# Kernel optimization log

Measured on AMD Instinct MI355X. Metric: run time of the kernel, lower is better.

Reference implementation:

```python
import jax, jax.numpy as jnp
import numpy as np

DIM = 1024        # BIGNET_DIM
GS = 16           # group_size
N_LAYERS = 18     # 6 blocks * 3 QLoRALinear
N_BLOCKS = 6
R = 32            # lora_dim
B = 32768         # flattened batch/tokens
LN_EPS = 1e-5


def _qlora_linear(x, qw, sc, b, la, lb):
    # Dequantize int4 weights: per-group (group_size=16 along in_features) scale.
    O, I = qw.shape
    w = (qw.astype(jnp.float32).reshape(O, I // GS, GS) * sc[:, :, None]).reshape(O, I)
    base = x @ w.T + b                      # [B, O] dequant-matmul
    lora = (x @ la.T) @ lb.T                # fp32 low-rank branch [B,R]->[B,O]
    return base + lora


def _layernorm(x, g, b):
    mu = jnp.mean(x, axis=-1, keepdims=True)
    var = jnp.mean((x - mu) ** 2, axis=-1, keepdims=True)
    return (x - mu) * jax.lax.rsqrt(var + LN_EPS) * g + b


def setup_inputs() -> dict:
    key = jax.random.key(0)
    ks = jax.random.split(key, 6)
    x = jax.random.normal(ks[0], (B, DIM), dtype=jnp.float32)
    # int4 codes in [-8, 7]
    qw = jax.random.randint(ks[1], (N_LAYERS, DIM, DIM), -8, 8, dtype=jnp.int32)
    # positive per-group scales (absmax/7-like magnitude)
    scales = jax.random.uniform(ks[2], (N_LAYERS, DIM, DIM // GS), dtype=jnp.float32,
                                minval=0.005, maxval=0.02)
    bias = 0.02 * jax.random.normal(ks[3], (N_LAYERS, DIM), dtype=jnp.float32)
    lora_a = (1.0 / np.sqrt(DIM)) * jax.random.normal(ks[4], (N_LAYERS, R, DIM), dtype=jnp.float32)
    # lora_b is zero-init in the module; use small random values so the branch is exercised
    lora_b = 0.01 * jax.random.normal(ks[5], (N_LAYERS, DIM, R), dtype=jnp.float32)
    ln_g = jnp.ones((N_BLOCKS - 1, DIM), dtype=jnp.float32)
    ln_b = jnp.zeros((N_BLOCKS - 1, DIM), dtype=jnp.float32)
    return {"x": x, "qw": qw, "scales": scales, "bias": bias,
            "lora_a": lora_a, "lora_b": lora_b, "ln_g": ln_g, "ln_b": ln_b}


def reference(x, qw, scales, bias, lora_a, lora_b, ln_g, ln_b):
    h = x
    for blk in range(N_BLOCKS):
        y = h
        for j in range(3):
            li = blk * 3 + j
            y = _qlora_linear(y, qw[li], scales[li], bias[li], lora_a[li], lora_b[li])
            if j < 2:
                y = jax.nn.relu(y)
        h = y + h                     # residual
        if blk < N_BLOCKS - 1:
            h = _layernorm(h, ln_g[blk], ln_b[blk])
    return h
```

## Files before the change

kernel.cpp:

```cpp
#include <hip/hip_runtime.h>
#include <cstdint>

typedef _Float16 f16;
typedef _Float16 f16x8 __attribute__((ext_vector_type(8)));
typedef _Float16 f16x4 __attribute__((ext_vector_type(4)));
typedef float    f32x4 __attribute__((ext_vector_type(4)));
typedef float    f32x16 __attribute__((ext_vector_type(16)));

#define DIMN 1024
#define BATCH 32768
#define NLAYERS 18
#define NBLOCKS 6

__device__ __forceinline__ void gl2lds16(const f16* g, const f16* l) {
    auto gp = (const __attribute__((address_space(1))) unsigned int*)(uintptr_t)g;
    auto lp = (__attribute__((address_space(3))) unsigned int*)(uintptr_t)l;
    __builtin_amdgcn_global_load_lds(gp, lp, 16, 0, 0);
}

__global__ void cvt_kernel(const float* __restrict__ x, f16* __restrict__ o) {
    int i = (blockIdx.x * 256 + threadIdx.x) * 4;
    float4 v = *(const float4*)&x[i];
    f16x4 r;
    r[0] = (f16)v.x; r[1] = (f16)v.y; r[2] = (f16)v.z; r[3] = (f16)v.w;
    *(f16x4*)&o[i] = r;
}

__global__ __launch_bounds__(256) void prep_w_kernel(
        const int* __restrict__ qw, const float* __restrict__ sc,
        const float* __restrict__ la, const float* __restrict__ lb,
        f16* __restrict__ W) {
    int b = blockIdx.x;
    int li = b >> 7;
    int og = (b & 127) << 3;
    __shared__ float lbs[8][32];
    int tid = threadIdx.x;
    lbs[tid >> 5][tid & 31] = lb[((size_t)li * 1024 + og + (tid >> 5)) * 32 + (tid & 31)];
    __syncthreads();

    int i0 = tid * 4;
    const float* laL = la + (size_t)li * 32 * 1024;
    float acc[8][4] = {};
    for (int r = 0; r < 32; ++r) {
        float4 lav = *(const float4*)&laL[r * 1024 + i0];
#pragma unroll
        for (int q = 0; q < 8; ++q) {
            float wv = lbs[q][r];
            acc[q][0] += wv * lav.x; acc[q][1] += wv * lav.y;
            acc[q][2] += wv * lav.z; acc[q][3] += wv * lav.w;
        }
    }
#pragma unroll
    for (int q = 0; q < 8; ++q) {
        size_t row = (size_t)li * 1024 + og + q;
        size_t rowbase = row * 1024;
        int4 code = *(const int4*)&qw[rowbase + i0];
        float scale = sc[row * 64 + (i0 >> 4)];
        f16x4 o;
        o[0] = (f16)((float)code.x * scale + acc[q][0]);
        o[1] = (f16)((float)code.y * scale + acc[q][1]);
        o[2] = (f16)((float)code.z * scale + acc[q][2]);
        o[3] = (f16)((float)code.w * scale + acc[q][3]);
        *(f16x4*)&W[rowbase + i0] = o;
    }
}

__global__ __launch_bounds__(512, 2) void gemm_kernel(
        const f16* __restrict__ A, const f16* __restrict__ W,
        const float* __restrict__ bias, f16* __restrict__ C, int relu) {
    __shared__ __align__(16) char smem[131072];

    int tid = threadIdx.x;
    int l = tid & 63, w = tid >> 6;
    int wm = w >> 2, wn = w & 3;
    int m_l = l & 31;
    int kg = l >> 5;

    int hb = blockIdx.x;
    int xcd = hb & 7, idx = hb >> 3;
    int mt = xcd * 16 + (idx >> 2);
    int nt = idx & 3;
    int bm = mt * 256, bn = nt * 256;

    int R0 = tid >> 3;
    int lgc = (tid & 7) ^ (R0 & 7);
    int hh = lgc >> 2, kch = lgc & 3;
    const f16* pA = A + (size_t)(bm + hh * 128 + R0) * 1024 + kch * 8;
    const f16* pB = W + (size_t)(bn + hh * 128 + R0) * 1024 + kch * 8;
    int ld0 = tid * 16;

#define STGA(SL, KT) do { \
    gl2lds16(pA + (KT) * 32, (const f16*)(smem + (SL) * 32768 + ld0)); \
    gl2lds16(pA + 65536 + (KT) * 32, (const f16*)(smem + (SL) * 32768 + 8192 + ld0)); } while (0)
#define STGB(SL, KT) do { \
    gl2lds16(pB + (KT) * 32, (const f16*)(smem + (SL) * 32768 + 16384 + ld0)); \
    gl2lds16(pB + 65536 + (KT) * 32, (const f16*)(smem + (SL) * 32768 + 24576 + ld0)); } while (0)

    int aoff[4], boff[2];
#pragma unroll
    for (int mf = 0; mf < 4; ++mf) aoff[mf] = (mf * 32 + m_l) * 128;
#pragma unroll
    for (int nf = 0; nf < 2; ++nf) boff[nf] = 16384 + ((wn & 1) * 64 + nf * 32 + m_l) * 128;
    int r7 = m_l & 7;
    int sa0 = ((wm * 4 + 0 + kg) ^ r7) * 16;
    int sa1 = ((wm * 4 + 2 + kg) ^ r7) * 16;
    int sb0 = (((wn >> 1) * 4 + 0 + kg) ^ r7) * 16;
    int sb1 = (((wn >> 1) * 4 + 2 + kg) ^ r7) * 16;

    f16x8 aE[4], bE[2], aO[4], bO[2];
    f32x16 acc[4][2] = {};

#define READS(DA, DB, SBASE, SA, SB) do { _Pragma("unroll") \
    for (int mf = 0; mf < 4; ++mf) DA[mf] = *(const f16x8*)(smem + (SBASE) + aoff[mf] + (SA)); \
    _Pragma("unroll") \
    for (int nf = 0; nf < 2; ++nf) DB[nf] = *(const f16x8*)(smem + (SBASE) + boff[nf] + (SB)); } while (0)

#define MMA8(AF, BF) do { _Pragma("unroll") \
    for (int mf = 0; mf < 4; ++mf) { _Pragma("unroll") \
      for (int nf = 0; nf < 2; ++nf) \
        acc[mf][nf] = __builtin_amdgcn_mfma_f32_32x32x16_f16(BF[nf], AF[mf], acc[mf][nf], 0, 0, 0); } } while (0)

#define WAITS do { \
    asm volatile("s_waitcnt vmcnt(4) lgkmcnt(6)" ::: "memory"); \
    __builtin_amdgcn_sched_barrier(0); \
    __builtin_amdgcn_s_barrier(); \
    __builtin_amdgcn_sched_barrier(0); } while (0)

#define PHASES(T4, DT) do { \
    int kp = ((T4) + (DT) + 3) & 31; \
     \
    READS(aO, bO, ((DT) & 3) * 32768, sa1, sb1); \
    STGA(((DT) + 3) & 3, kp); \
    WAITS; \
    __builtin_amdgcn_s_setprio(1); \
    MMA8(aE, bE); \
    __builtin_amdgcn_s_setprio(0); \
    __builtin_amdgcn_sched_barrier(0); \
     \
    READS(aE, bE, (((DT) + 1) & 3) * 32768, sa0, sb0); \
    STGB(((DT) + 3) & 3, kp); \
    WAITS; \
    __builtin_amdgcn_s_setprio(1); \
    MMA8(aO, bO); \
    __builtin_amdgcn_s_setprio(0); \
    __builtin_amdgcn_sched_barrier(0); \
  } while (0)

    STGA(0, 0); STGB(0, 0);
    STGA(1, 1); STGB(1, 1);
    STGA(2, 2); STGB(2, 2);
    asm volatile("s_waitcnt vmcnt(4)" ::: "memory");
    __builtin_amdgcn_s_barrier();
    READS(aE, bE, 0, sa0, sb0);

#pragma unroll 1
    for (int t4 = 0; t4 < 32; t4 += 4) {
        PHASES(t4, 0);
        PHASES(t4, 1);
        PHASES(t4, 2);
        PHASES(t4, 3);
    }

    __syncthreads();
    f16* Cs = (f16*)smem;
    float4 bsv[2][4];
#pragma unroll
    for (int nf = 0; nf < 2; ++nf)
#pragma unroll
        for (int g = 0; g < 4; ++g)
            bsv[nf][g] = *(const float4*)&bias[bn + wn * 64 + nf * 32 + g * 8 + kg * 4];

    int c8 = (tid & 31) * 8, rr = tid >> 5;
#pragma unroll
    for (int pass = 0; pass < 2; ++pass) {
        if (wm == pass) {
#pragma unroll
            for (int mf = 0; mf < 4; ++mf) {
                int row = mf * 32 + m_l;
#pragma unroll
                for (int nf = 0; nf < 2; ++nf)
#pragma unroll
                    for (int g = 0; g < 4; ++g) {
                        float4 vb = bsv[nf][g];
                        float v0 = acc[mf][nf][g * 4 + 0] + vb.x;
                        float v1 = acc[mf][nf][g * 4 + 1] + vb.y;
                        float v2 = acc[mf][nf][g * 4 + 2] + vb.z;
                        float v3 = acc[mf][nf][g * 4 + 3] + vb.w;
                        if (relu) {
                            v0 = fmaxf(v0, 0.f); v1 = fmaxf(v1, 0.f);
                            v2 = fmaxf(v2, 0.f); v3 = fmaxf(v3, 0.f);
                        }
                        f16x4 pk;
                        pk[0] = (f16)v0; pk[1] = (f16)v1; pk[2] = (f16)v2; pk[3] = (f16)v3;
                        *(f16x4*)&Cs[row * 264 + wn * 64 + nf * 32 + g * 8 + kg * 4] = pk;
                    }
            }
        }
        __syncthreads();
#pragma unroll
        for (int it = 0; it < 8; ++it) {
            int rowr = rr + it * 16;
            f16x8 val = *(const f16x8*)&Cs[rowr * 264 + c8];
            *(f16x8*)&C[(size_t)(bm + pass * 128 + rowr) * 1024 + bn + c8] = val;
        }
        if (pass == 0) __syncthreads();
    }
}

__global__ void res_ln_kernel(const f16* __restrict__ y, f16* __restrict__ h,
                              const float* __restrict__ g, const float* __restrict__ b,
                              float* __restrict__ outF, int mode) {
    int row = blockIdx.x;
    int tid = threadIdx.x;
    int c0 = tid * 4;
    const f16* yr = y + (size_t)row * DIMN;
    f16* hr = h + (size_t)row * DIMN;

    f16x4 yv = *(const f16x4*)&yr[c0];
    f16x4 hv = *(const f16x4*)&hr[c0];
    float v[4];
    float s = 0.f, sq = 0.f;
#pragma unroll
    for (int i = 0; i < 4; ++i) {
        v[i] = (float)yv[i] + (float)hv[i];
        s += v[i]; sq += v[i] * v[i];
    }
#pragma unroll
    for (int o = 32; o > 0; o >>= 1) {
        s += __shfl_xor(s, o);
        sq += __shfl_xor(sq, o);
    }
    __shared__ float red[8];
    int wv = tid >> 6, ln = tid & 63;
    if (ln == 0) { red[wv] = s; red[4 + wv] = sq; }
    __syncthreads();
    float S1 = red[0] + red[1] + red[2] + red[3];
    float S2 = red[4] + red[5] + red[6] + red[7];
    float mu = S1 * (1.f / 1024.f);
    float var = S2 * (1.f / 1024.f) - mu * mu;
    float rs = rsqrtf(var + 1e-5f);

    if (mode == 0) {
        float4 gv = *(const float4*)&g[c0];
        float4 bv = *(const float4*)&b[c0];
        f16x4 outv;
        outv[0] = (f16)((v[0] - mu) * rs * gv.x + bv.x);
        outv[1] = (f16)((v[1] - mu) * rs * gv.y + bv.y);
        outv[2] = (f16)((v[2] - mu) * rs * gv.z + bv.z);
        outv[3] = (f16)((v[3] - mu) * rs * gv.w + bv.w);
        *(f16x4*)&hr[c0] = outv;
    } else {
        float4 ov;
        ov.x = v[0]; ov.y = v[1]; ov.z = v[2]; ov.w = v[3];
        *(float4*)&outF[(size_t)row * DIMN + c0] = ov;
    }
}

extern "C" void kernel_launch(void* const* d_in, const int* in_sizes, int n_in,
                              void* d_out, int out_size, void* d_ws, size_t ws_size,
                              hipStream_t stream) {
    const float* x    = (const float*)d_in[0];
    const int*   qw   = (const int*)d_in[1];
    const float* sc   = (const float*)d_in[2];
    const float* bias = (const float*)d_in[3];
    const float* la   = (const float*)d_in[4];
    const float* lb   = (const float*)d_in[5];
    const float* lng  = (const float*)d_in[6];
    const float* lnb  = (const float*)d_in[7];
    float* out = (float*)d_out;

    char* ws = (char*)d_ws;
    f16* Weff = (f16*)ws;
    f16* H    = (f16*)(ws + (size_t)37748736);
    f16* P    = (f16*)(ws + (size_t)37748736 + 67108864);
    f16* Q    = (f16*)d_out;

    cvt_kernel<<<BATCH * DIMN / (256 * 4), 256, 0, stream>>>(x, H);
    prep_w_kernel<<<NLAYERS * 128, 256, 0, stream>>>(qw, sc, la, lb, Weff);

    for (int blk = 0; blk < NBLOCKS; ++blk) {
        for (int j = 0; j < 3; ++j) {
            int li = blk * 3 + j;
            const f16* in = (j == 0) ? H : ((j == 1) ? P : Q);
            f16* o = (j == 1) ? Q : P;
            gemm_kernel<<<512, 512, 0, stream>>>(
                in, Weff + ((size_t)li << 20), bias + li * 1024, o, (j < 2) ? 1 : 0);
        }
        int lnidx = (blk < 5) ? blk : 4;
        res_ln_kernel<<<BATCH, 256, 0, stream>>>(
            P, H, lng + lnidx * 1024, lnb + lnidx * 1024, out, (blk == 5) ? 1 : 0);
    }
}
```

Before: 1.716 ms.

## Fuse residual add into GEMM epilogue and halve barriers in main loop

```diff
diff --git a/kernel.cpp b/kernel.cpp
--- a/kernel.cpp
+++ b/kernel.cpp
@@ -67,7 +67,8 @@
 
 __global__ __launch_bounds__(512, 2) void gemm_kernel(
         const f16* __restrict__ A, const f16* __restrict__ W,
-        const float* __restrict__ bias, f16* __restrict__ C, int relu) {
+        const float* __restrict__ bias, f16* __restrict__ C,
+        const f16* __restrict__ Hres, int op) {
     __shared__ __align__(16) char smem[131072];
 
     int tid = threadIdx.x;
@@ -120,26 +121,22 @@
       for (int nf = 0; nf < 2; ++nf) \
         acc[mf][nf] = __builtin_amdgcn_mfma_f32_32x32x16_f16(BF[nf], AF[mf], acc[mf][nf], 0, 0, 0); } } while (0)
 
-#define WAITS do { \
-    asm volatile("s_waitcnt vmcnt(4) lgkmcnt(6)" ::: "memory"); \
-    __builtin_amdgcn_sched_barrier(0); \
-    __builtin_amdgcn_s_barrier(); \
-    __builtin_amdgcn_sched_barrier(0); } while (0)
-
-#define PHASES(T4, DT) do { \
+#define PHASE(T4, DT) do { \
     int kp = ((T4) + (DT) + 3) & 31; \
-     \
     READS(aO, bO, ((DT) & 3) * 32768, sa1, sb1); \
     STGA(((DT) + 3) & 3, kp); \
-    WAITS; \
+    asm volatile("s_waitcnt lgkmcnt(6)" ::: "memory"); \
+    __builtin_amdgcn_sched_barrier(0); \
     __builtin_amdgcn_s_setprio(1); \
     MMA8(aE, bE); \
     __builtin_amdgcn_s_setprio(0); \
     __builtin_amdgcn_sched_barrier(0); \
-     \
     READS(aE, bE, (((DT) + 1) & 3) * 32768, sa0, sb0); \
     STGB(((DT) + 3) & 3, kp); \
-    WAITS; \
+    asm volatile("s_waitcnt vmcnt(4) lgkmcnt(6)" ::: "memory"); \
+    __builtin_amdgcn_sched_barrier(0); \
+    __builtin_amdgcn_s_barrier(); \
+    __builtin_amdgcn_sched_barrier(0); \
     __builtin_amdgcn_s_setprio(1); \
     MMA8(aO, bO); \
     __builtin_amdgcn_s_setprio(0); \
@@ -155,12 +152,13 @@
 
 #pragma unroll 1
     for (int t4 = 0; t4 < 32; t4 += 4) {
-        PHASES(t4, 0);
-        PHASES(t4, 1);
-        PHASES(t4, 2);
-        PHASES(t4, 3);
-    }
-
+        PHASE(t4, 0);
+        PHASE(t4, 1);
+        PHASE(t4, 2);
+        PHASE(t4, 3);
+    }
+
+    asm volatile("s_waitcnt vmcnt(0)" ::: "memory");
     __syncthreads();
     f16* Cs = (f16*)smem;
     float4 bsv[2][4];
@@ -186,13 +184,13 @@
                         float v1 = acc[mf][nf][g * 4 + 1] + vb.y;
                         float v2 = acc[mf][nf][g * 4 + 2] + vb.z;
                         float v3 = acc[mf][nf][g * 4 + 3] + vb.w;
-                        if (relu) {
+                        if (op == 1) {
                             v0 = fmaxf(v0, 0.f); v1 = fmaxf(v1, 0.f);
                             v2 = fmaxf(v2, 0.f); v3 = fmaxf(v3, 0.f);
                         }
                         f16x4 pk;
                         pk[0] = (f16)v0; pk[1] = (f16)v1; pk[2] = (f16)v2; pk[3] = (f16)v3;
-                        *(f16x4*)&Cs[row * 264 + wn * 64 + nf * 32 + g * 8 + kg * 4] = pk;
+                        *(f16x4*)&Cs[row * 268 + wn * 64 + nf * 32 + g * 8 + kg * 4] = pk;
                     }
             }
         }
@@ -200,8 +198,19 @@
 #pragma unroll
         for (int it = 0; it < 8; ++it) {
             int rowr = rr + it * 16;
-            f16x8 val = *(const f16x8*)&Cs[rowr * 264 + c8];
-            *(f16x8*)&C[(size_t)(bm + pass * 128 + rowr) * 1024 + bn + c8] = val;
+            f16x4 lo = *(const f16x4*)&Cs[rowr * 268 + c8];
+            f16x4 hi = *(const f16x4*)&Cs[rowr * 268 + c8 + 4];
+            f16x8 val;
+            val[0] = lo[0]; val[1] = lo[1]; val[2] = lo[2]; val[3] = lo[3];
+            val[4] = hi[0]; val[5] = hi[1]; val[6] = hi[2]; val[7] = hi[3];
+            size_t gidx = (size_t)(bm + pass * 128 + rowr) * 1024 + bn + c8;
+            if (op == 2) {
+                f16x8 hv = *(const f16x8*)&Hres[gidx];
+#pragma unroll
+                for (int q = 0; q < 8; ++q)
+                    val[q] = (f16)((float)val[q] + (float)hv[q]);
+            }
+            *(f16x8*)&C[gidx] = val;
         }
         if (pass == 0) __syncthreads();
     }
@@ -217,12 +226,21 @@
     f16* hr = h + (size_t)row * DIMN;
 
     f16x4 yv = *(const f16x4*)&yr[c0];
-    f16x4 hv = *(const f16x4*)&hr[c0];
+    if (mode == 1) {
+        f16x4 hv = *(const f16x4*)&hr[c0];
+        float4 ov;
+        ov.x = (float)yv[0] + (float)hv[0];
+        ov.y = (float)yv[1] + (float)hv[1];
+        ov.z = (float)yv[2] + (float)hv[2];
+        ov.w = (float)yv[3] + (float)hv[3];
+        *(float4*)&outF[(size_t)row * DIMN + c0] = ov;
+        return;
+    }
     float v[4];
     float s = 0.f, sq = 0.f;
 #pragma unroll
     for (int i = 0; i < 4; ++i) {
-        v[i] = (float)yv[i] + (float)hv[i];
+        v[i] = (float)yv[i];
         s += v[i]; sq += v[i] * v[i];
     }
 #pragma unroll
@@ -240,20 +258,14 @@
     float var = S2 * (1.f / 1024.f) - mu * mu;
     float rs = rsqrtf(var + 1e-5f);
 
-    if (mode == 0) {
-        float4 gv = *(const float4*)&g[c0];
-        float4 bv = *(const float4*)&b[c0];
-        f16x4 outv;
-        outv[0] = (f16)((v[0] - mu) * rs * gv.x + bv.x);
-        outv[1] = (f16)((v[1] - mu) * rs * gv.y + bv.y);
-        outv[2] = (f16)((v[2] - mu) * rs * gv.z + bv.z);
-        outv[3] = (f16)((v[3] - mu) * rs * gv.w + bv.w);
-        *(f16x4*)&hr[c0] = outv;
-    } else {
-        float4 ov;
-        ov.x = v[0]; ov.y = v[1]; ov.z = v[2]; ov.w = v[3];
-        *(float4*)&outF[(size_t)row * DIMN + c0] = ov;
-    }
+    float4 gv = *(const float4*)&g[c0];
+    float4 bv = *(const float4*)&b[c0];
+    f16x4 outv;
+    outv[0] = (f16)((v[0] - mu) * rs * gv.x + bv.x);
+    outv[1] = (f16)((v[1] - mu) * rs * gv.y + bv.y);
+    outv[2] = (f16)((v[2] - mu) * rs * gv.z + bv.z);
+    outv[3] = (f16)((v[3] - mu) * rs * gv.w + bv.w);
+    *(f16x4*)&hr[c0] = outv;
 }
 
 extern "C" void kernel_launch(void* const* d_in, const int* in_sizes, int n_in,
@@ -283,8 +295,9 @@
             int li = blk * 3 + j;
             const f16* in = (j == 0) ? H : ((j == 1) ? P : Q);
             f16* o = (j == 1) ? Q : P;
+            int op = (j < 2) ? 1 : ((blk < 5) ? 2 : 0);
             gemm_kernel<<<512, 512, 0, stream>>>(
-                in, Weff + ((size_t)li << 20), bias + li * 1024, o, (j < 2) ? 1 : 0);
+                in, Weff + ((size_t)li << 20), bias + li * 1024, o, H, op);
         }
         int lnidx = (blk < 5) ? blk : 4;
         res_ln_kernel<<<BATCH, 256, 0, stream>>>(
```

After: 1.802 ms. 5.0% more time.
